# Kernel optimization log

Hardware: AMD Instinct MI355X
Metric: run time of the kernel (lower is better)

## Reference

```python
import jax, jax.numpy as jnp
import numpy as np

B, S, D, H = 2, 2048, 1024, 16
HD = D // H  # 64


def setup_inputs() -> dict:
    key = jax.random.key(0)
    ks = jax.random.split(key, 12)
    scale = 1.0 / np.sqrt(D)
    inp = {
        "input_query": jax.random.normal(ks[0], (B, S, D), jnp.float32),
        "input_key": jax.random.normal(ks[1], (B, S, D), jnp.float32),
        "input_value": jax.random.normal(ks[2], (B, S, D), jnp.float32),
        "mask": jax.random.randint(ks[3], (B, 1, S), 0, 2, jnp.int32),
        # torch nn.Linear params: y = x @ W.T + b, W shape (out, in)
        "wq": jax.random.uniform(ks[4], (D, D), jnp.float32, -scale, scale),
        "bq": jax.random.uniform(ks[5], (D,), jnp.float32, -scale, scale),
        "wk": jax.random.uniform(ks[6], (D, D), jnp.float32, -scale, scale),
        "bk": jax.random.uniform(ks[7], (D,), jnp.float32, -scale, scale),
        "wv": jax.random.uniform(ks[8], (D, D), jnp.float32, -scale, scale),
        "bv": jax.random.uniform(ks[9], (D,), jnp.float32, -scale, scale),
        "wo": jax.random.uniform(ks[10], (D, D), jnp.float32, -scale, scale),
        "bo": jax.random.uniform(ks[11], (D,), jnp.float32, -scale, scale),
    }
    return inp


def _split_heads(x):
    # (B, S, D) -> (B, H, S, HD)
    return x.reshape(B, S, H, HD).transpose(0, 2, 1, 3)


def reference(input_query, input_key, input_value, mask, wq, bq, wk, bk, wv, bv, wo, bo):
    q = _split_heads(input_query @ wq.T + bq)
    k = _split_heads(input_key @ wk.T + bk)
    v = _split_heads(input_value @ wv.T + bv)

    # scaled dot-product attention (materializes [B,H,S,S] as the original does)
    scores = jnp.einsum("bhqd,bhkd->bhqk", q, k) / np.sqrt(HD).astype(np.float32)
    # mask: (B, 1, S) -> unsqueeze(1) -> (B, 1, 1, S); fill -1e9 where mask == 0
    m = mask[:, None, :, :]
    scores = jnp.where(m == 0, jnp.float32(-1e9), scores)
    p_attn = jax.nn.softmax(scores, axis=-1)  # dropout is identity (rate 0 / eval)

    out = jnp.einsum("bhqk,bhkd->bhqd", p_attn, v)
    out = out.transpose(0, 2, 1, 3).reshape(B, S, D)
    return out @ wo.T + bo
```

## Files before the change

### kernel.cpp

```cpp
#include <hip/hip_runtime.h>
#include <math.h>

#define BB 2
#define SS 2048
#define DD 1024
#define HH 16
#define HD 64

typedef short short8 __attribute__((ext_vector_type(8)));
typedef float floatx4 __attribute__((ext_vector_type(4)));

__device__ inline ushort f2bf_rne(float x) {
    union { float f; unsigned u; } v; v.f = x;
    unsigned r = v.u + 0x7FFFu + ((v.u >> 16) & 1u);
    return (ushort)(r >> 16);
}
__device__ inline float bf2f(ushort h) {
    union { unsigned u; float f; } v; v.u = ((unsigned)h) << 16;
    return v.f;
}
__device__ inline ushort f2bf_trunc(float x) {
    union { float f; unsigned u; } v; v.f = x;
    return (ushort)(v.u >> 16);
}

__global__ __launch_bounds__(256)
void convert_bf16(const float* __restrict__ xq, const float* __restrict__ xk,
                  const float* __restrict__ xv,
                  const float* __restrict__ wq, const float* __restrict__ wk,
                  const float* __restrict__ wv, const float* __restrict__ wo,
                  ushort* __restrict__ Xq, ushort* __restrict__ Xk,
                  ushort* __restrict__ Xv,
                  ushort* __restrict__ Wq, ushort* __restrict__ Wk,
                  ushort* __restrict__ Wv, ushort* __restrict__ Wo)
{
    const int z = blockIdx.z;
    const size_t i = ((size_t)blockIdx.x * 256 + threadIdx.x) * 8;

    const float* src;
    ushort* dst;
    size_t off;
    if (z < 3) {
        src = (z == 0) ? xq : (z == 1) ? xk : xv;
        dst = (z == 0) ? Xq : (z == 1) ? Xk : Xv;
        off = i;
    } else {
        const int seg = (int)(i >> 20);
        off = i & ((1u << 20) - 1);
        src = (seg == 0) ? wq : (seg == 1) ? wk : (seg == 2) ? wv : wo;
        dst = (seg == 0) ? Wq : (seg == 1) ? Wk : (seg == 2) ? Wv : Wo;
    }
    float x[8];
    *(float4*)&x[0] = *(const float4*)(src + off);
    *(float4*)&x[4] = *(const float4*)(src + off + 4);
    short8 h8;
#pragma unroll
    for (int j = 0; j < 8; ++j) h8[j] = (short)f2bf_rne(x[j]);
    *(short8*)&dst[off] = h8;
}

#define LDK 40

__global__ __launch_bounds__(256, 3)
void qkv_gemm(const ushort* __restrict__ Xq, const ushort* __restrict__ Xk,
              const ushort* __restrict__ Xv,
              const ushort* __restrict__ Wq, const ushort* __restrict__ Wk,
              const ushort* __restrict__ Wv,
              const float* __restrict__ bq, const float* __restrict__ bk,
              const float* __restrict__ bv,
              ushort* __restrict__ Qo, ushort* __restrict__ Ko,
              ushort* __restrict__ Vo, float qscale)
{
    __shared__ ushort Alds[128][LDK];
    __shared__ ushort Blds[128][LDK];

    const int z   = blockIdx.z;
    const int tid = threadIdx.x;

    const ushort* X    = (z == 0) ? Xq : (z == 1) ? Xk : Xv;
    const ushort* W    = (z == 0) ? Wq : (z == 1) ? Wk : Wv;
    const float*  bias = (z == 0) ? bq : (z == 1) ? bk : bv;
    const float   osc  = (z == 0) ? qscale : 1.0f;

    const int lane = tid & 63;
    const int wave = tid >> 6;
    const int wr = wave >> 1;
    const int wc = wave & 1;
    const int lt = lane & 15;
    const int lq = lane >> 4;
    const int m0 = blockIdx.y * 128;
    const int n0 = blockIdx.x * 128;

    floatx4 acc[4][4];
#pragma unroll
    for (int mi = 0; mi < 4; ++mi)
#pragma unroll
        for (int ni = 0; ni < 4; ++ni) acc[mi][ni] = (floatx4)0.0f;

    const int srow = tid >> 1;
    const int sks  = (tid & 1) << 4;
    const size_t xrow = (size_t)(m0 + srow) * DD;
    const size_t wrow = (size_t)(n0 + srow) * DD;

    for (int k0 = 0; k0 < DD; k0 += 32) {
        const short8 a0 = *(const short8*)(X + xrow + k0 + sks);
        const short8 a1 = *(const short8*)(X + xrow + k0 + sks + 8);
        const short8 b0 = *(const short8*)(W + wrow + k0 + sks);
        const short8 b1 = *(const short8*)(W + wrow + k0 + sks + 8);

        __syncthreads();
        *(short8*)&Alds[srow][sks]     = a0;
        *(short8*)&Alds[srow][sks + 8] = a1;
        *(short8*)&Blds[srow][sks]     = b0;
        *(short8*)&Blds[srow][sks + 8] = b1;
        __syncthreads();

        short8 af[4], bf_[4];
#pragma unroll
        for (int mi = 0; mi < 4; ++mi)
            af[mi] = *(const short8*)&Alds[wr * 64 + mi * 16 + lt][lq * 8];
#pragma unroll
        for (int ni = 0; ni < 4; ++ni)
            bf_[ni] = *(const short8*)&Blds[wc * 64 + ni * 16 + lt][lq * 8];

#pragma unroll
        for (int mi = 0; mi < 4; ++mi)
#pragma unroll
            for (int ni = 0; ni < 4; ++ni)
                acc[mi][ni] = __builtin_amdgcn_mfma_f32_16x16x32_bf16(af[mi], bf_[ni], acc[mi][ni], 0, 0, 0);
    }

    float bb[4];
#pragma unroll
    for (int ni = 0; ni < 4; ++ni) bb[ni] = bias[n0 + wc * 64 + ni * 16 + lt];

    if (z <= 1) {
        ushort* C = z ? Ko : Qo;
#pragma unroll
        for (int mi = 0; mi < 4; ++mi)
#pragma unroll
            for (int ni = 0; ni < 4; ++ni) {
                const int n = n0 + wc * 64 + ni * 16 + lt;
                const int h = n >> 6;
#pragma unroll
                for (int r = 0; r < 4; ++r) {
                    const int m = m0 + wr * 64 + mi * 16 + lq * 4 + r;
                    const int b = m >> 11;
                    const int s = m & (SS - 1);
                    C[(size_t)((b * HH + h) * SS + s) * HD + (n & 63)] =
                        f2bf_rne((acc[mi][ni][r] + bb[ni]) * osc);
                }
            }
    } else {
#pragma unroll
        for (int mi = 0; mi < 4; ++mi)
#pragma unroll
            for (int ni = 0; ni < 4; ++ni) {
                const int n = n0 + wc * 64 + ni * 16 + lt;
                const int h = n >> 6;
                const int mb = m0 + wr * 64 + mi * 16 + lq * 4;
                const int b = mb >> 11;
                const int s = mb & (SS - 1);
                ushort4 pack;
                pack.x = f2bf_rne(acc[mi][ni][0] + bb[ni]);
                pack.y = f2bf_rne(acc[mi][ni][1] + bb[ni]);
                pack.z = f2bf_rne(acc[mi][ni][2] + bb[ni]);
                pack.w = f2bf_rne(acc[mi][ni][3] + bb[ni]);
                *(ushort4*)&Vo[(size_t)((b * HH + h) * HD + (n & 63)) * SS + s] = pack;
            }
    }
}

#define ATQ 128
#define LDV 68
#define LDP 68

__global__ __launch_bounds__(256, 2)
void attn_mfma(const ushort* __restrict__ Qb, const ushort* __restrict__ Kb,
               const ushort* __restrict__ Vt, const int* __restrict__ mask,
               ushort* __restrict__ Ob)
{
    __shared__ __align__(16) ushort Klds[2][64][LDV];
    __shared__ __align__(16) ushort Vlds[2][64][LDV];
    __shared__ __align__(16) ushort Pw[4][32][LDP];

    const int tid  = threadIdx.x;
    const int lane = tid & 63;
    const int wave = tid >> 6;
    const int lt = lane & 15;
    const int lq = lane >> 4;

    const int bid    = blockIdx.x;
    const int xcd    = bid & 7;
    const int slot   = bid >> 3;
    const int bhloc  = slot >> 4;
    const int qi     = slot & 15;
    const int bh     = xcd * 4 + bhloc;
    const int b      = bh >> 4;
    const int q0     = qi * ATQ;

    const size_t sbase = (size_t)bh * SS * HD;
    const size_t vbase = (size_t)bh * HD * SS;

    short8 ones;
#pragma unroll
    for (int j = 0; j < 8; ++j) ones[j] = (short)0x3F80;

    short8 qb[2][2];
#pragma unroll
    for (int mt = 0; mt < 2; ++mt)
#pragma unroll
        for (int ks = 0; ks < 2; ++ks)
            qb[mt][ks] = *(const short8*)(Qb + sbase +
                          (size_t)(q0 + wave * 32 + mt * 16 + lt) * HD + ks * 32 + lq * 8);

    floatx4 oacc[2][4];
#pragma unroll
    for (int mt = 0; mt < 2; ++mt)
#pragma unroll
        for (int dt = 0; dt < 4; ++dt) oacc[mt][dt] = (floatx4)0.0f;

    float lrow[2][4];
#pragma unroll
    for (int mt = 0; mt < 2; ++mt)
#pragma unroll
        for (int r = 0; r < 4; ++r) lrow[mt][r] = 0.0f;

    const int srow = tid >> 2;
    const int sp8  = (tid & 3) << 4;

    short8 kr0, kr1, vr0, vr1;
    int mcur[4], mnxt[4];

    {
        const size_t koff = sbase + (size_t)srow * HD + sp8;
        kr0 = *(const short8*)(Kb + koff);
        kr1 = *(const short8*)(Kb + koff + 8);
        const size_t voff = vbase + (size_t)srow * SS + sp8;
        vr0 = *(const short8*)(Vt + voff);
        vr1 = *(const short8*)(Vt + voff + 8);
#pragma unroll
        for (int nt = 0; nt < 4; ++nt) mcur[nt] = mask[b * SS + nt * 16 + lt];
        *(short8*)&Klds[0][srow][sp8]     = kr0;
        *(short8*)&Klds[0][srow][sp8 + 8] = kr1;
        *(short8*)&Vlds[0][srow][sp8]     = vr0;
        *(short8*)&Vlds[0][srow][sp8 + 8] = vr1;
    }

    const int NT = SS / 64;
    for (int kt = 0; kt < NT; ++kt) {
        const int cur = kt & 1;
        __syncthreads();

        if (kt + 1 < NT) {
            const int k0n = (kt + 1) * 64;
            const size_t koff = sbase + (size_t)(k0n + srow) * HD + sp8;
            kr0 = *(const short8*)(Kb + koff);
            kr1 = *(const short8*)(Kb + koff + 8);
            const size_t voff = vbase + (size_t)srow * SS + k0n + sp8;
            vr0 = *(const short8*)(Vt + voff);
            vr1 = *(const short8*)(Vt + voff + 8);
#pragma unroll
            for (int nt = 0; nt < 4; ++nt) mnxt[nt] = mask[b * SS + k0n + nt * 16 + lt];
        }

        floatx4 sacc[2][4];
#pragma unroll
        for (int mt = 0; mt < 2; ++mt)
#pragma unroll
            for (int nt = 0; nt < 4; ++nt) sacc[mt][nt] = (floatx4)0.0f;

#pragma unroll
        for (int nt = 0; nt < 4; ++nt) {
            const short8 kf0 = *(const short8*)&Klds[cur][nt * 16 + lt][lq * 8];
            const short8 kf1 = *(const short8*)&Klds[cur][nt * 16 + lt][32 + lq * 8];
#pragma unroll
            for (int mt = 0; mt < 2; ++mt) {
                sacc[mt][nt] = __builtin_amdgcn_mfma_f32_16x16x32_bf16(qb[mt][0], kf0, sacc[mt][nt], 0, 0, 0);
                sacc[mt][nt] = __builtin_amdgcn_mfma_f32_16x16x32_bf16(qb[mt][1], kf1, sacc[mt][nt], 0, 0, 0);
            }
        }

#pragma unroll
        for (int mt = 0; mt < 2; ++mt)
#pragma unroll
            for (int nt = 0; nt < 4; ++nt)
#pragma unroll
                for (int r = 0; r < 4; ++r) {
                    const float p = (mcur[nt] == 0) ? 0.0f : exp2f(sacc[mt][nt][r]);
                    Pw[wave][mt * 16 + lq * 4 + r][nt * 16 + lt] = f2bf_trunc(p);
                }

        short8 pa[2][2];
#pragma unroll
        for (int mt = 0; mt < 2; ++mt)
#pragma unroll
            for (int ks = 0; ks < 2; ++ks)
                pa[mt][ks] = *(const short8*)&Pw[wave][mt * 16 + lt][ks * 32 + lq * 8];

#pragma unroll
        for (int mt = 0; mt < 2; ++mt) {
            floatx4 a = (floatx4)0.0f;
            a = __builtin_amdgcn_mfma_f32_16x16x32_bf16(pa[mt][0], ones, a, 0, 0, 0);
            a = __builtin_amdgcn_mfma_f32_16x16x32_bf16(pa[mt][1], ones, a, 0, 0, 0);
#pragma unroll
            for (int r = 0; r < 4; ++r) lrow[mt][r] += a[r];
        }

#pragma unroll
        for (int dt = 0; dt < 4; ++dt) {
            const short8 vf0 = *(const short8*)&Vlds[cur][dt * 16 + lt][lq * 8];
            const short8 vf1 = *(const short8*)&Vlds[cur][dt * 16 + lt][32 + lq * 8];
#pragma unroll
            for (int mt = 0; mt < 2; ++mt) {
                oacc[mt][dt] = __builtin_amdgcn_mfma_f32_16x16x32_bf16(pa[mt][0], vf0, oacc[mt][dt], 0, 0, 0);
                oacc[mt][dt] = __builtin_amdgcn_mfma_f32_16x16x32_bf16(pa[mt][1], vf1, oacc[mt][dt], 0, 0, 0);
            }
        }

        if (kt + 1 < NT) {
            const int nxt = cur ^ 1;
            *(short8*)&Klds[nxt][srow][sp8]     = kr0;
            *(short8*)&Klds[nxt][srow][sp8 + 8] = kr1;
            *(short8*)&Vlds[nxt][srow][sp8]     = vr0;
            *(short8*)&Vlds[nxt][srow][sp8 + 8] = vr1;
#pragma unroll
            for (int nt = 0; nt < 4; ++nt) mcur[nt] = mnxt[nt];
        }
    }

    const int h = bh & 15;
#pragma unroll
    for (int mt = 0; mt < 2; ++mt) {
        float linv[4];
#pragma unroll
        for (int r = 0; r < 4; ++r) linv[r] = 1.0f / lrow[mt][r];
#pragma unroll
        for (int dt = 0; dt < 4; ++dt)
#pragma unroll
            for (int r = 0; r < 4; ++r) {
                const int row = q0 + wave * 32 + mt * 16 + lq * 4 + r;
                Ob[(size_t)(b * SS + row) * DD + h * HD + dt * 16 + lt] =
                    f2bf_rne(oacc[mt][dt][r] * linv[r]);
            }
    }
}

__global__ __launch_bounds__(256, 3)
void o_gemm(const ushort* __restrict__ A, const ushort* __restrict__ B,
            const float* __restrict__ bias, float* __restrict__ out)
{
    __shared__ ushort sA[128][LDK];
    __shared__ ushort sB[64][LDK];

    const int tid  = threadIdx.x;
    const int lane = tid & 63;
    const int wave = tid >> 6;
    const int wr = wave >> 1;
    const int wc = wave & 1;
    const int lt = lane & 15;
    const int lq = lane >> 4;
    const int m0 = blockIdx.y * 128;
    const int n0 = blockIdx.x * 64;

    floatx4 acc[4][2];
#pragma unroll
    for (int mi = 0; mi < 4; ++mi)
#pragma unroll
        for (int ni = 0; ni < 2; ++ni) acc[mi][ni] = (floatx4)0.0f;

    const int arow = tid >> 1, apart = (tid & 1) << 4;
    const int brow = tid >> 2, bpart = (tid & 3) << 3;

    for (int k0 = 0; k0 < DD; k0 += 32) {
        const size_t aoff = (size_t)(m0 + arow) * DD + k0 + apart;
        const size_t boff = (size_t)(n0 + brow) * DD + k0 + bpart;
        const short8 a0 = *(const short8*)(A + aoff);
        const short8 a1 = *(const short8*)(A + aoff + 8);
        const short8 b0 = *(const short8*)(B + boff);

        __syncthreads();
        *(short8*)&sA[arow][apart]     = a0;
        *(short8*)&sA[arow][apart + 8] = a1;
        *(short8*)&sB[brow][bpart]     = b0;
        __syncthreads();

        short8 af[4], bf_[2];
#pragma unroll
        for (int mi = 0; mi < 4; ++mi)
            af[mi] = *(const short8*)&sA[wr * 64 + mi * 16 + lt][lq * 8];
#pragma unroll
        for (int ni = 0; ni < 2; ++ni)
            bf_[ni] = *(const short8*)&sB[wc * 32 + ni * 16 + lt][lq * 8];

#pragma unroll
        for (int mi = 0; mi < 4; ++mi)
#pragma unroll
            for (int ni = 0; ni < 2; ++ni)
                acc[mi][ni] = __builtin_amdgcn_mfma_f32_16x16x32_bf16(af[mi], bf_[ni], acc[mi][ni], 0, 0, 0);
    }

#pragma unroll
    for (int mi = 0; mi < 4; ++mi)
#pragma unroll
        for (int ni = 0; ni < 2; ++ni) {
            const int n = n0 + wc * 32 + ni * 16 + lt;
            const float bb = bias[n];
#pragma unroll
            for (int r = 0; r < 4; ++r) {
                const int m = m0 + wr * 64 + mi * 16 + lq * 4 + r;
                out[(size_t)m * DD + n] = acc[mi][ni][r] + bb;
            }
        }
}

extern "C" void kernel_launch(void* const* d_in, const int* in_sizes, int n_in,
                              void* d_out, int out_size, void* d_ws, size_t ws_size,
                              hipStream_t stream) {
    const float* xq   = (const float*)d_in[0];
    const float* xk   = (const float*)d_in[1];
    const float* xv   = (const float*)d_in[2];
    const int*   mask = (const int*)d_in[3];
    const float* wq   = (const float*)d_in[4];
    const float* bq   = (const float*)d_in[5];
    const float* wk   = (const float*)d_in[6];
    const float* bk   = (const float*)d_in[7];
    const float* wv   = (const float*)d_in[8];
    const float* bv   = (const float*)d_in[9];
    const float* wo   = (const float*)d_in[10];
    const float* bo   = (const float*)d_in[11];
    float* out = (float*)d_out;

    const size_t n = (size_t)BB * SS * DD;
    const size_t w1 = (size_t)DD * DD;

    ushort* Xqb = (ushort*)d_ws;
    ushort* Xkb = Xqb + n;
    ushort* Xvb = Xkb + n;
    ushort* Kb  = Xvb + n;
    ushort* Vt  = Kb + n;
    ushort* Wob = Vt + n;
    ushort* Ob  = Xqb;

    ushort* Qb  = (ushort*)out;
    ushort* Wqb = Qb + n;
    ushort* Wkb = Wqb + w1;
    ushort* Wvb = Wkb + w1;

    const float qscale = 0.125f * 1.44269504088896340736f;

    dim3 gc(2048, 1, 4);
    convert_bf16<<<gc, 256, 0, stream>>>(xq, xk, xv, wq, wk, wv, wo,
                                         Xqb, Xkb, Xvb, Wqb, Wkb, Wvb, Wob);

    dim3 g1(DD / 128, (BB * SS) / 128, 3);
    qkv_gemm<<<g1, 256, 0, stream>>>(Xqb, Xkb, Xvb, Wqb, Wkb, Wvb,
                                     bq, bk, bv, Qb, Kb, Vt, qscale);

    attn_mfma<<<dim3(512), 256, 0, stream>>>(Qb, Kb, Vt, mask, Ob);

    dim3 g2(DD / 64, (BB * SS) / 128);
    o_gemm<<<g2, 256, 0, stream>>>(Ob, Wob, bo, out);
}
```

Baseline: 254.4 us.

## Use 32x32 MFMA transposed scores and fold mask into V and row-sum

Rewrites the attention inner loop to use 32x32x16 bf16 MFMAs that compute S^T (K as the A operand), so the exp'd probabilities can be packed with v_cvt_pk_bf16 and permlane32_swap straight into register operands. This removes the per-tile LDS round trip for P. The mask moves out of the loop: V rows are zeroed by the mask in the QKV GEMM epilogue, and the row sum uses a bf16 mask vector held in LDS as the MFMA B operand. The changes cut LDS traffic and VALU work, but they tie correctness to the mask being exactly 0/1 and assume no row is fully masked.

```diff
diff --git a/kernel.cpp b/kernel.cpp
--- a/kernel.cpp
+++ b/kernel.cpp
@@ -9,6 +9,8 @@
 
 typedef short short8 __attribute__((ext_vector_type(8)));
 typedef float floatx4 __attribute__((ext_vector_type(4)));
+typedef float floatx16 __attribute__((ext_vector_type(16)));
+typedef unsigned int uintx2 __attribute__((ext_vector_type(2)));
 
 __device__ inline ushort f2bf_rne(float x) {
     union { float f; unsigned u; } v; v.f = x;
@@ -19,9 +21,15 @@
     union { unsigned u; float f; } v; v.u = ((unsigned)h) << 16;
     return v.f;
 }
-__device__ inline ushort f2bf_trunc(float x) {
-    union { float f; unsigned u; } v; v.f = x;
-    return (ushort)(v.u >> 16);
+__device__ inline unsigned cvt_pk_bf16(float lo, float hi) {
+    unsigned r;
+    asm("v_cvt_pk_bf16_f32 %0, %1, %2" : "=v"(r) : "v"(lo), "v"(hi));
+    return r;
+}
+__device__ inline short8 mk_pf(uintx2 x, uintx2 y) {
+    union { unsigned u[4]; short8 s; } t;
+    t.u[0] = x[0]; t.u[1] = y[0]; t.u[2] = x[1]; t.u[3] = y[1];
+    return t.s;
 }
 
 __global__ __launch_bounds__(256)
@@ -67,7 +75,7 @@
               const ushort* __restrict__ Wq, const ushort* __restrict__ Wk,
               const ushort* __restrict__ Wv,
               const float* __restrict__ bq, const float* __restrict__ bk,
-              const float* __restrict__ bv,
+              const float* __restrict__ bv, const int* __restrict__ mask,
               ushort* __restrict__ Qo, ushort* __restrict__ Ko,
               ushort* __restrict__ Vo, float qscale)
 {
@@ -130,9 +138,9 @@
                 acc[mi][ni] = __builtin_amdgcn_mfma_f32_16x16x32_bf16(af[mi], bf_[ni], acc[mi][ni], 0, 0, 0);
     }
 
-    float bb[4];
-#pragma unroll
-    for (int ni = 0; ni < 4; ++ni) bb[ni] = bias[n0 + wc * 64 + ni * 16 + lt];
+    float bbv[4];
+#pragma unroll
+    for (int ni = 0; ni < 4; ++ni) bbv[ni] = bias[n0 + wc * 64 + ni * 16 + lt];
 
     if (z <= 1) {
         ushort* C = z ? Ko : Qo;
@@ -148,32 +156,35 @@
                     const int b = m >> 11;
                     const int s = m & (SS - 1);
                     C[(size_t)((b * HH + h) * SS + s) * HD + (n & 63)] =
-                        f2bf_rne((acc[mi][ni][r] + bb[ni]) * osc);
+                        f2bf_rne((acc[mi][ni][r] + bbv[ni]) * osc);
                 }
             }
     } else {
 #pragma unroll
-        for (int mi = 0; mi < 4; ++mi)
+        for (int mi = 0; mi < 4; ++mi) {
+            const int mb  = m0 + wr * 64 + mi * 16 + lq * 4;
+            const int bb_ = mb >> 11;
+            const int s   = mb & (SS - 1);
+            const int4 mm = *(const int4*)(mask + bb_ * SS + s);
+            const float mf0 = (float)mm.x, mf1 = (float)mm.y;
+            const float mf2 = (float)mm.z, mf3 = (float)mm.w;
 #pragma unroll
             for (int ni = 0; ni < 4; ++ni) {
                 const int n = n0 + wc * 64 + ni * 16 + lt;
                 const int h = n >> 6;
-                const int mb = m0 + wr * 64 + mi * 16 + lq * 4;
-                const int b = mb >> 11;
-                const int s = mb & (SS - 1);
                 ushort4 pack;
-                pack.x = f2bf_rne(acc[mi][ni][0] + bb[ni]);
-                pack.y = f2bf_rne(acc[mi][ni][1] + bb[ni]);
-                pack.z = f2bf_rne(acc[mi][ni][2] + bb[ni]);
-                pack.w = f2bf_rne(acc[mi][ni][3] + bb[ni]);
-                *(ushort4*)&Vo[(size_t)((b * HH + h) * HD + (n & 63)) * SS + s] = pack;
+                pack.x = f2bf_rne((acc[mi][ni][0] + bbv[ni]) * mf0);
+                pack.y = f2bf_rne((acc[mi][ni][1] + bbv[ni]) * mf1);
+                pack.z = f2bf_rne((acc[mi][ni][2] + bbv[ni]) * mf2);
+                pack.w = f2bf_rne((acc[mi][ni][3] + bbv[ni]) * mf3);
+                *(ushort4*)&Vo[(size_t)((bb_ * HH + h) * HD + (n & 63)) * SS + s] = pack;
             }
+        }
     }
 }
 
 #define ATQ 128
 #define LDV 68
-#define LDP 68
 
 __global__ __launch_bounds__(256, 2)
 void attn_mfma(const ushort* __restrict__ Qb, const ushort* __restrict__ Kb,
@@ -182,13 +193,13 @@
 {
     __shared__ __align__(16) ushort Klds[2][64][LDV];
     __shared__ __align__(16) ushort Vlds[2][64][LDV];
-    __shared__ __align__(16) ushort Pw[4][32][LDP];
+    __shared__ __align__(16) ushort Mlds[SS];
 
     const int tid  = threadIdx.x;
     const int lane = tid & 63;
     const int wave = tid >> 6;
-    const int lt = lane & 15;
-    const int lq = lane >> 4;
+    const int ll   = lane & 31;
+    const int hi   = lane >> 5;
 
     const int bid    = blockIdx.x;
     const int xcd    = bid & 7;
@@ -202,35 +213,36 @@
     const size_t sbase = (size_t)bh * SS * HD;
     const size_t vbase = (size_t)bh * HD * SS;
 
-    short8 ones;
-#pragma unroll
-    for (int j = 0; j < 8; ++j) ones[j] = (short)0x3F80;
-
-    short8 qb[2][2];
-#pragma unroll
-    for (int mt = 0; mt < 2; ++mt)
-#pragma unroll
-        for (int ks = 0; ks < 2; ++ks)
-            qb[mt][ks] = *(const short8*)(Qb + sbase +
-                          (size_t)(q0 + wave * 32 + mt * 16 + lt) * HD + ks * 32 + lq * 8);
-
-    floatx4 oacc[2][4];
-#pragma unroll
-    for (int mt = 0; mt < 2; ++mt)
-#pragma unroll
-        for (int dt = 0; dt < 4; ++dt) oacc[mt][dt] = (floatx4)0.0f;
-
-    float lrow[2][4];
-#pragma unroll
-    for (int mt = 0; mt < 2; ++mt)
-#pragma unroll
-        for (int r = 0; r < 4; ++r) lrow[mt][r] = 0.0f;
+    {
+        const int4 m0 = *(const int4*)(mask + b * SS + tid * 8);
+        const int4 m1 = *(const int4*)(mask + b * SS + tid * 8 + 4);
+        short8 mv;
+        mv[0] = m0.x ? (short)0x3F80 : (short)0;
+        mv[1] = m0.y ? (short)0x3F80 : (short)0;
+        mv[2] = m0.z ? (short)0x3F80 : (short)0;
+        mv[3] = m0.w ? (short)0x3F80 : (short)0;
+        mv[4] = m1.x ? (short)0x3F80 : (short)0;
+        mv[5] = m1.y ? (short)0x3F80 : (short)0;
+        mv[6] = m1.z ? (short)0x3F80 : (short)0;
+        mv[7] = m1.w ? (short)0x3F80 : (short)0;
+        *(short8*)&Mlds[tid * 8] = mv;
+    }
+
+    short8 qf[4];
+    const size_t qrow = sbase + (size_t)(q0 + wave * 32 + ll) * HD;
+#pragma unroll
+    for (int dc = 0; dc < 4; ++dc)
+        qf[dc] = *(const short8*)(Qb + qrow + dc * 16 + hi * 8);
+
+    floatx16 oacc[2];
+    oacc[0] = (floatx16)0.0f;
+    oacc[1] = (floatx16)0.0f;
+    floatx16 lacc = (floatx16)0.0f;
 
     const int srow = tid >> 2;
     const int sp8  = (tid & 3) << 4;
 
     short8 kr0, kr1, vr0, vr1;
-    int mcur[4], mnxt[4];
 
     {
         const size_t koff = sbase + (size_t)srow * HD + sp8;
@@ -239,8 +251,6 @@
         const size_t voff = vbase + (size_t)srow * SS + sp8;
         vr0 = *(const short8*)(Vt + voff);
         vr1 = *(const short8*)(Vt + voff + 8);
-#pragma unroll
-        for (int nt = 0; nt < 4; ++nt) mcur[nt] = mask[b * SS + nt * 16 + lt];
         *(short8*)&Klds[0][srow][sp8]     = kr0;
         *(short8*)&Klds[0][srow][sp8 + 8] = kr1;
         *(short8*)&Vlds[0][srow][sp8]     = vr0;
@@ -260,61 +270,48 @@
             const size_t voff = vbase + (size_t)srow * SS + k0n + sp8;
             vr0 = *(const short8*)(Vt + voff);
             vr1 = *(const short8*)(Vt + voff + 8);
-#pragma unroll
-            for (int nt = 0; nt < 4; ++nt) mnxt[nt] = mask[b * SS + k0n + nt * 16 + lt];
-        }
-
-        floatx4 sacc[2][4];
-#pragma unroll
-        for (int mt = 0; mt < 2; ++mt)
-#pragma unroll
-            for (int nt = 0; nt < 4; ++nt) sacc[mt][nt] = (floatx4)0.0f;
-
-#pragma unroll
-        for (int nt = 0; nt < 4; ++nt) {
-            const short8 kf0 = *(const short8*)&Klds[cur][nt * 16 + lt][lq * 8];
-            const short8 kf1 = *(const short8*)&Klds[cur][nt * 16 + lt][32 + lq * 8];
-#pragma unroll
-            for (int mt = 0; mt < 2; ++mt) {
-                sacc[mt][nt] = __builtin_amdgcn_mfma_f32_16x16x32_bf16(qb[mt][0], kf0, sacc[mt][nt], 0, 0, 0);
-                sacc[mt][nt] = __builtin_amdgcn_mfma_f32_16x16x32_bf16(qb[mt][1], kf1, sacc[mt][nt], 0, 0, 0);
+        }
+
+#pragma unroll
+        for (int sub = 0; sub < 2; ++sub) {
+            floatx16 sacc = (floatx16)0.0f;
+#pragma unroll
+            for (int dc = 0; dc < 4; ++dc) {
+                const short8 kf = *(const short8*)&Klds[cur][sub * 32 + ll][dc * 16 + hi * 8];
+                sacc = __builtin_amdgcn_mfma_f32_32x32x16_bf16(kf, qf[dc], sacc, 0, 0, 0);
             }
-        }
-
-#pragma unroll
-        for (int mt = 0; mt < 2; ++mt)
-#pragma unroll
-            for (int nt = 0; nt < 4; ++nt)
-#pragma unroll
-                for (int r = 0; r < 4; ++r) {
-                    const float p = (mcur[nt] == 0) ? 0.0f : exp2f(sacc[mt][nt][r]);
-                    Pw[wave][mt * 16 + lq * 4 + r][nt * 16 + lt] = f2bf_trunc(p);
-                }
-
-        short8 pa[2][2];
-#pragma unroll
-        for (int mt = 0; mt < 2; ++mt)
-#pragma unroll
-            for (int ks = 0; ks < 2; ++ks)
-                pa[mt][ks] = *(const short8*)&Pw[wave][mt * 16 + lt][ks * 32 + lq * 8];
-
-#pragma unroll
-        for (int mt = 0; mt < 2; ++mt) {
-            floatx4 a = (floatx4)0.0f;
-            a = __builtin_amdgcn_mfma_f32_16x16x32_bf16(pa[mt][0], ones, a, 0, 0, 0);
-            a = __builtin_amdgcn_mfma_f32_16x16x32_bf16(pa[mt][1], ones, a, 0, 0, 0);
-#pragma unroll
-            for (int r = 0; r < 4; ++r) lrow[mt][r] += a[r];
-        }
-
-#pragma unroll
-        for (int dt = 0; dt < 4; ++dt) {
-            const short8 vf0 = *(const short8*)&Vlds[cur][dt * 16 + lt][lq * 8];
-            const short8 vf1 = *(const short8*)&Vlds[cur][dt * 16 + lt][32 + lq * 8];
-#pragma unroll
-            for (int mt = 0; mt < 2; ++mt) {
-                oacc[mt][dt] = __builtin_amdgcn_mfma_f32_16x16x32_bf16(pa[mt][0], vf0, oacc[mt][dt], 0, 0, 0);
-                oacc[mt][dt] = __builtin_amdgcn_mfma_f32_16x16x32_bf16(pa[mt][1], vf1, oacc[mt][dt], 0, 0, 0);
+
+            float p[16];
+#pragma unroll
+            for (int r = 0; r < 16; ++r) p[r] = exp2f(sacc[r]);
+
+            const unsigned pk_a = cvt_pk_bf16(p[0],  p[1]);
+            const unsigned pk_b = cvt_pk_bf16(p[2],  p[3]);
+            const unsigned pk_c = cvt_pk_bf16(p[4],  p[5]);
+            const unsigned pk_d = cvt_pk_bf16(p[6],  p[7]);
+            const unsigned pk_e = cvt_pk_bf16(p[8],  p[9]);
+            const unsigned pk_f = cvt_pk_bf16(p[10], p[11]);
+            const unsigned pk_g = cvt_pk_bf16(p[12], p[13]);
+            const unsigned pk_h = cvt_pk_bf16(p[14], p[15]);
+            const uintx2 s1 = __builtin_amdgcn_permlane32_swap(pk_a, pk_c, false, false);
+            const uintx2 s2 = __builtin_amdgcn_permlane32_swap(pk_b, pk_d, false, false);
+            const uintx2 s3 = __builtin_amdgcn_permlane32_swap(pk_e, pk_g, false, false);
+            const uintx2 s4 = __builtin_amdgcn_permlane32_swap(pk_f, pk_h, false, false);
+            const short8 pf0 = mk_pf(s1, s2);
+            const short8 pf1 = mk_pf(s3, s4);
+
+            const int kbase = kt * 64 + sub * 32;
+            const short8 mf0 = *(const short8*)&Mlds[kbase + hi * 8];
+            const short8 mf1 = *(const short8*)&Mlds[kbase + 16 + hi * 8];
+            lacc = __builtin_amdgcn_mfma_f32_32x32x16_bf16(pf0, mf0, lacc, 0, 0, 0);
+            lacc = __builtin_amdgcn_mfma_f32_32x32x16_bf16(pf1, mf1, lacc, 0, 0, 0);
+
+#pragma unroll
+            for (int dn = 0; dn < 2; ++dn) {
+                const short8 vf0 = *(const short8*)&Vlds[cur][dn * 32 + ll][sub * 32 + hi * 8];
+                const short8 vf1 = *(const short8*)&Vlds[cur][dn * 32 + ll][sub * 32 + 16 + hi * 8];
+                oacc[dn] = __builtin_amdgcn_mfma_f32_32x32x16_bf16(pf0, vf0, oacc[dn], 0, 0, 0);
+                oacc[dn] = __builtin_amdgcn_mfma_f32_32x32x16_bf16(pf1, vf1, oacc[dn], 0, 0, 0);
             }
         }
 
@@ -324,26 +321,21 @@
             *(short8*)&Klds[nxt][srow][sp8 + 8] = kr1;
             *(short8*)&Vlds[nxt][srow][sp8]     = vr0;
             *(short8*)&Vlds[nxt][srow][sp8 + 8] = vr1;
-#pragma unroll
-            for (int nt = 0; nt < 4; ++nt) mcur[nt] = mnxt[nt];
         }
     }
 
     const int h = bh & 15;
-#pragma unroll
-    for (int mt = 0; mt < 2; ++mt) {
-        float linv[4];
-#pragma unroll
-        for (int r = 0; r < 4; ++r) linv[r] = 1.0f / lrow[mt][r];
-#pragma unroll
-        for (int dt = 0; dt < 4; ++dt)
-#pragma unroll
-            for (int r = 0; r < 4; ++r) {
-                const int row = q0 + wave * 32 + mt * 16 + lq * 4 + r;
-                Ob[(size_t)(b * SS + row) * DD + h * HD + dt * 16 + lt] =
-                    f2bf_rne(oacc[mt][dt][r] * linv[r]);
-            }
-    }
+    float linv[16];
+#pragma unroll
+    for (int r = 0; r < 16; ++r) linv[r] = 1.0f / lacc[r];
+#pragma unroll
+    for (int dn = 0; dn < 2; ++dn)
+#pragma unroll
+        for (int r = 0; r < 16; ++r) {
+            const int q = q0 + wave * 32 + (r & 3) + 8 * (r >> 2) + 4 * hi;
+            Ob[(size_t)(b * SS + q) * DD + h * HD + dn * 32 + ll] =
+                f2bf_rne(oacc[dn][r] * linv[r]);
+        }
 }
 
 __global__ __launch_bounds__(256, 3)
@@ -455,7 +447,7 @@
 
     dim3 g1(DD / 128, (BB * SS) / 128, 3);
     qkv_gemm<<<g1, 256, 0, stream>>>(Xqb, Xkb, Xvb, Wqb, Wkb, Wvb,
-                                     bq, bk, bv, Qb, Kb, Vt, qscale);
+                                     bq, bk, bv, mask, Qb, Kb, Vt, qscale);
 
     attn_mfma<<<dim3(512), 256, 0, stream>>>(Qb, Kb, Vt, mask, Ob);
 
```

Result: faster. 238.4 us (-6.3%).
